# Kernel optimization log

Measured on AMD Instinct MI355X. Metric: run time of the kernel, lower is better.

## Reference

```python
import jax, jax.numpy as jnp
import numpy as np

N_NODES = 100000
N_EDGES = 1000000
D_FEAT = 128
N_ACTIONS = 64


def setup_inputs() -> dict:
    key = jax.random.key(0)
    ks = jax.random.split(key, 8)
    return {
        "x": jax.random.normal(ks[0], (N_NODES, D_FEAT), dtype=jnp.float32),
        "edge_index": jax.random.randint(ks[1], (2, N_EDGES), 0, N_NODES, dtype=jnp.int64),
        "W_gcn": jax.random.normal(ks[2], (D_FEAT, D_FEAT), dtype=jnp.float32) / np.sqrt(D_FEAT),
        "b_gcn": jax.random.normal(ks[3], (D_FEAT,), dtype=jnp.float32) * 0.02,
        "W_high": jax.random.normal(ks[4], (D_FEAT, N_ACTIONS), dtype=jnp.float32) / np.sqrt(D_FEAT),
        "b_high": jax.random.normal(ks[5], (N_ACTIONS,), dtype=jnp.float32) * 0.02,
        "W_low": jax.random.normal(ks[6], (D_FEAT, N_ACTIONS), dtype=jnp.float32) / np.sqrt(D_FEAT),
        "b_low": jax.random.normal(ks[7], (N_ACTIONS,), dtype=jnp.float32) * 0.02,
    }


def gcn_conv(x, edge_index, W, b):
    """PyG GCNConv: add self-loops, symmetric normalization, aggregate, linear."""
    n = x.shape[0]
    loops = jnp.arange(n, dtype=edge_index.dtype)
    src = jnp.concatenate([edge_index[0], loops])  # message sources
    dst = jnp.concatenate([edge_index[1], loops])  # message targets
    # degree of each target node (edge weight 1, incl. self-loop)
    deg = jax.ops.segment_sum(jnp.ones(src.shape[0], dtype=x.dtype), dst, num_segments=n)
    dinv = jax.lax.rsqrt(deg)  # deg >= 1 thanks to self-loops
    norm = dinv[src] * dinv[dst]  # [E+N]
    h = x @ W  # [N, D] dense transform first (cheaper than transforming messages)
    agg = jax.ops.segment_sum(h[src] * norm[:, None], dst, num_segments=n)
    return agg + b


def reference(x, edge_index, W_gcn, b_gcn, W_high, b_high, W_low, b_low):
    h = gcn_conv(x, edge_index, W_gcn, b_gcn)  # [N, D]
    high = h @ W_high + b_high  # [N, A]
    low = h @ W_low + b_low     # [N, A]
    return (high, low)
```

## Files before the change

### kernel.cpp

```cpp
#include <hip/hip_runtime.h>


#define BLOCK 256
#define SB 512
#define NB_MAX 784
#define SLOT 2048
#define CHUNK_MAX 2048

typedef _Float16 half8 __attribute__((ext_vector_type(8)));
typedef _Float16 half4 __attribute__((ext_vector_type(4)));
typedef float f32x4 __attribute__((ext_vector_type(4)));


__global__ __launch_bounds__(BLOCK) void k_prep(const float* __restrict__ Wg,
                                                const float* __restrict__ Wh,
                                                const float* __restrict__ Wl,
                                                const float* __restrict__ bg,
                                                const float* __restrict__ bh,
                                                const float* __restrict__ bl,
                                                _Float16* __restrict__ WfT,
                                                float* __restrict__ bf,
                                                int* __restrict__ cursor,
                                                int NB) {
    int b = blockIdx.x;
    if (b < 16) {
        int r = b * 8 + (threadIdx.x >> 5);
        int c0 = (threadIdx.x & 31) * 4;
        float a0 = 0.f, a1 = 0.f, a2 = 0.f, a3 = 0.f;
        for (int j = 0; j < 128; j++) {
            float wg = Wg[r * 128 + j];
            float4 wc;
            if (c0 < 64) wc = *(const float4*)(Wh + j * 64 + c0);
            else         wc = *(const float4*)(Wl + j * 64 + (c0 - 64));
            a0 += wg * wc.x; a1 += wg * wc.y; a2 += wg * wc.z; a3 += wg * wc.w;
        }
        WfT[(size_t)(c0 + 0) * 128 + r] = (_Float16)a0;
        WfT[(size_t)(c0 + 1) * 128 + r] = (_Float16)a1;
        WfT[(size_t)(c0 + 2) * 128 + r] = (_Float16)a2;
        WfT[(size_t)(c0 + 3) * 128 + r] = (_Float16)a3;
    } else {
        int c = threadIdx.x;
        if (c < 128) {
            float acc = (c < 64) ? bh[c] : bl[c - 64];
            for (int j = 0; j < 128; j++) {
                float wc = (c < 64) ? Wh[j * 64 + c] : Wl[j * 64 + (c - 64)];
                acc += bg[j] * wc;
            }
            bf[c] = acc;
        }
        for (int i = threadIdx.x; i < NB; i += BLOCK) cursor[i] = i * SLOT;
    }
}


__global__ __launch_bounds__(BLOCK) void k_scatter(const int* __restrict__ src,
                                                   const int* __restrict__ dst, int E,
                                                   int* __restrict__ cursor,
                                                   int2* __restrict__ ebuf, int NB) {
    __shared__ int2 stash[CHUNK_MAX];
    __shared__ int hist[NB_MAX];
    __shared__ int cur[NB_MAX];
    int blk = blockIdx.x;
    int chunk = (E + SB - 1) / SB;
    int e0 = blk * chunk, e1 = min(E, e0 + chunk);
    int m = e1 - e0;

    for (int i = threadIdx.x; i < NB; i += BLOCK) hist[i] = 0;
    __syncthreads();
    for (int i = threadIdx.x; i < m; i += BLOCK) {
        int d = dst[e0 + i], s = src[e0 + i];
        stash[i] = make_int2(d, s);
        atomicAdd(&hist[d >> 7], 1);
    }
    __syncthreads();
    for (int i = threadIdx.x; i < NB; i += BLOCK) {
        int h = hist[i];
        cur[i] = h ? atomicAdd(&cursor[i], h) : 0;
    }
    __syncthreads();
    for (int i = threadIdx.x; i < m; i += BLOCK) {
        int2 p = stash[i];
        int pos = atomicAdd(&cur[p.x >> 7], 1);
        ebuf[pos] = p;
    }
}


__global__ __launch_bounds__(BLOCK) void k_node(const int2* __restrict__ ebuf,
                                                const int* __restrict__ cursor,
                                                const float* __restrict__ x,
                                                int2* __restrict__ off2,
                                                float* __restrict__ dinv,
                                                int* __restrict__ csr,
                                                _Float16* __restrict__ xh,
                                                int n) {
    __shared__ int cnt[128];
    __shared__ int pre[128];
    __shared__ int cur[128];
    int bkt = blockIdx.x;
    int t = threadIdx.x;
    int node0 = bkt << 7;
    int nn = min(128, n - node0);
    int eb0 = bkt * SLOT;
    int eb1 = cursor[bkt];

    if (t < 128) cnt[t] = 0;
    __syncthreads();
    for (int e = eb0 + t; e < eb1; e += BLOCK)
        atomicAdd(&cnt[ebuf[e].x & 127], 1);
    __syncthreads();
    if (t < 128) pre[t] = cnt[t];
    __syncthreads();
    for (int ofs = 1; ofs < 128; ofs <<= 1) {
        int v = (t < 128 && t >= ofs) ? pre[t - ofs] : 0;
        __syncthreads();
        if (t < 128) pre[t] += v;
        __syncthreads();
    }
    if (t < 128) cur[t] = pre[t] - cnt[t];
    __syncthreads();
    if (t < nn) {
        off2[node0 + t] = make_int2(eb0 + cur[t], eb0 + pre[t]);
        dinv[node0 + t] = rsqrtf((float)(cnt[t] + 1));
    }
    for (int e = eb0 + t; e < eb1; e += BLOCK) {
        int2 p = ebuf[e];
        int pos = atomicAdd(&cur[p.x & 127], 1);
        csr[eb0 + pos] = p.y;
    }
    const float4* xr = (const float4*)(x + (size_t)node0 * 128);
    half4* xw = (half4*)(xh + (size_t)node0 * 128);
    for (int idx = t; idx < nn * 32; idx += BLOCK) {
        int row = idx >> 5;
        float dvL = rsqrtf((float)(cnt[row] + 1));
        float4 v = xr[idx];
        half4 o;
        o.x = (_Float16)(dvL * v.x); o.y = (_Float16)(dvL * v.y);
        o.z = (_Float16)(dvL * v.z); o.w = (_Float16)(dvL * v.w);
        xw[idx] = o;
    }
}


__global__ __launch_bounds__(BLOCK) void k_gf(const int2* __restrict__ off2,
                                              const int* __restrict__ csr,
                                              const float* __restrict__ dinv,
                                              const _Float16* __restrict__ xh,
                                              const _Float16* __restrict__ WfT,
                                              const float* __restrict__ bf,
                                              float* __restrict__ out, int n) {
    __shared__ _Float16 lds[64 * 128];
    int wave = threadIdx.x >> 6;
    int lane = threadIdx.x & 63;
    int g = lane >> 4;
    int sl = lane & 15;
    int T0 = blockIdx.x * 64;
    int wrow0 = wave * 16;
    int lbase = g << 4;

    for (int p = 0; p < 4; p++) {
        int r = wrow0 + p * 4 + g;
        int d = T0 + r;
        int dc = min(d, n - 1);
        int2 oe = off2[dc];
        float dv = dinv[dc];
        int beg = oe.x;
        int end = (d < n) ? oe.y : oe.x;
        half8 sv = *(const half8*)(xh + (size_t)dc * 128 + sl * 8);
        float acc[8];
#pragma unroll
        for (int k = 0; k < 8; k++) acc[k] = (float)sv[k];

        for (int b0 = beg; b0 < end; b0 += 16) {
            int take = min(16, end - b0);
            int s = 0;
            if (sl < take) s = csr[b0 + sl];
            for (int j = 0; j < take; j += 4) {
                int se0 = __shfl(s, lbase + j);
                int se1 = __shfl(s, lbase + ((j + 1) & 15));
                int se2 = __shfl(s, lbase + ((j + 2) & 15));
                int se3 = __shfl(s, lbase + ((j + 3) & 15));
                float m1 = (j + 1 < take) ? 1.f : 0.f;
                float m2 = (j + 2 < take) ? 1.f : 0.f;
                float m3 = (j + 3 < take) ? 1.f : 0.f;
                half8 v0 = *(const half8*)(xh + (size_t)se0 * 128 + sl * 8);
                half8 v1 = *(const half8*)(xh + (size_t)se1 * 128 + sl * 8);
                half8 v2 = *(const half8*)(xh + (size_t)se2 * 128 + sl * 8);
                half8 v3 = *(const half8*)(xh + (size_t)se3 * 128 + sl * 8);
#pragma unroll
                for (int k = 0; k < 8; k++)
                    acc[k] += (float)v0[k] + m1 * (float)v1[k]
                            + m2 * (float)v2[k] + m3 * (float)v3[k];
            }
        }
        half8 o;
#pragma unroll
        for (int k = 0; k < 8; k++) o[k] = (_Float16)(dv * acc[k]);
        *(half8*)(lds + (size_t)r * 128 + ((sl ^ (r & 7)) * 8)) = o;
    }

    int l15 = sl, lk = g;
    half8 a[4];
    {
        int r = wrow0 + l15;
#pragma unroll
        for (int kk = 0; kk < 4; kk++) {
            int ch = (kk * 4 + lk) ^ (l15 & 7);
            a[kk] = *(const half8*)(lds + (size_t)r * 128 + ch * 8);
        }
    }
    f32x4 acc[8];
#pragma unroll
    for (int cf = 0; cf < 8; cf++) acc[cf] = (f32x4){0.f, 0.f, 0.f, 0.f};
#pragma unroll
    for (int kk = 0; kk < 4; kk++) {
#pragma unroll
        for (int cf = 0; cf < 8; cf++) {
            half8 bfr = *(const half8*)(WfT + (size_t)(cf * 16 + l15) * 128 + kk * 32 + lk * 8);
            acc[cf] = __builtin_amdgcn_mfma_f32_16x16x32_f16(a[kk], bfr, acc[cf], 0, 0, 0);
        }
    }
#pragma unroll
    for (int cf = 0; cf < 8; cf++) {
        int c = cf * 16 + l15;
        float bv = bf[c];
        size_t cbase = (c < 64) ? (size_t)c : (size_t)n * 64 + (size_t)(c - 64);
        int r0 = T0 + wrow0 + lk * 4;
#pragma unroll
        for (int j = 0; j < 4; j++) {
            int rr = r0 + j;
            if (rr < n) out[cbase + (size_t)rr * 64] = acc[cf][j] + bv;
        }
    }
}

extern "C" void kernel_launch(void* const* d_in, const int* in_sizes, int n_in,
                              void* d_out, int out_size, void* d_ws, size_t ws_size,
                              hipStream_t stream) {
    const float* x  = (const float*)d_in[0];
    const int*   ei = (const int*)d_in[1];
    const float* Wg = (const float*)d_in[2];
    const float* bg = (const float*)d_in[3];
    const float* Wh = (const float*)d_in[4];
    const float* bh = (const float*)d_in[5];
    const float* Wl = (const float*)d_in[6];
    const float* bl = (const float*)d_in[7];
    float* out = (float*)d_out;

    int n = in_sizes[0] / 128;
    int E = in_sizes[1] / 2;
    const int* src = ei;
    const int* dst = ei + E;
    int NB = (n + 127) >> 7;

#define WS_TAKE(ptr, type, count)                                        \
    ptr = (type*)wsp;                                                    \
    wsp = (char*)(((size_t)(wsp + (size_t)(count) * sizeof(type)) + 255) \
                  & ~(size_t)255)

    char* wsp = (char*)d_ws;
    int*      cursor; WS_TAKE(cursor, int,      NB_MAX);
    int2*     ebuf;   WS_TAKE(ebuf,   int2,     (size_t)NB_MAX * SLOT);
    int2*     off2;   WS_TAKE(off2,   int2,     n);
    float*    dinv;   WS_TAKE(dinv,   float,    n);
    int*      csr;    WS_TAKE(csr,    int,      (size_t)NB_MAX * SLOT);
    _Float16* WfT;    WS_TAKE(WfT,    _Float16, 128 * 128);
    float*    bf;     WS_TAKE(bf,     float,    128);
    _Float16* xh;     WS_TAKE(xh,     _Float16, (size_t)n * 128);

    k_prep<<<17, BLOCK, 0, stream>>>(Wg, Wh, Wl, bg, bh, bl, WfT, bf, cursor, NB);
    k_scatter<<<SB, BLOCK, 0, stream>>>(src, dst, E, cursor, ebuf, NB);
    k_node<<<NB, BLOCK, 0, stream>>>(ebuf, cursor, x, off2, dinv, csr, xh, n);
    k_gf<<<(n + 63) / 64, BLOCK, 0, stream>>>(off2, csr, dinv, xh, WfT, bf, out, n);
}
```

Measured before the change: 245.3 us.

## Fuse prep into scatter, pack edges, restructure gather to wave-per-node

Merges the weight-prep kernel into the scatter kernel and initializes cursors with a memset. Edge records are packed into one int (src plus local dst in the high bits), which halves the bucket buffer traffic, and the dinv array is dropped in favour of recomputing rsqrt from the degree. The aggregation now gives each node a whole 64-lane wave that reads 2 halves per lane, uses readlane to broadcast neighbor indices, and prefetches the next node's CSR chunk. The packing assumes node ids fit in 20 bits, and the wider per-node gather may waste lanes on low-degree nodes.

```diff
diff --git a/kernel.cpp b/kernel.cpp
--- a/kernel.cpp
+++ b/kernel.cpp
@@ -5,23 +5,20 @@
 #define SB 512
 #define NB_MAX 784
 #define SLOT 2048
-#define CHUNK_MAX 2048
 
 typedef _Float16 half8 __attribute__((ext_vector_type(8)));
 typedef _Float16 half4 __attribute__((ext_vector_type(4)));
+typedef _Float16 half2v __attribute__((ext_vector_type(2)));
 typedef float f32x4 __attribute__((ext_vector_type(4)));
 
 
-__global__ __launch_bounds__(BLOCK) void k_prep(const float* __restrict__ Wg,
-                                                const float* __restrict__ Wh,
-                                                const float* __restrict__ Wl,
-                                                const float* __restrict__ bg,
-                                                const float* __restrict__ bh,
-                                                const float* __restrict__ bl,
-                                                _Float16* __restrict__ WfT,
-                                                float* __restrict__ bf,
-                                                int* __restrict__ cursor,
-                                                int NB) {
+__global__ __launch_bounds__(BLOCK) void k_scatter(
+    const int* __restrict__ src, const int* __restrict__ dst, int E,
+    const float* __restrict__ Wg, const float* __restrict__ Wh,
+    const float* __restrict__ Wl, const float* __restrict__ bg,
+    const float* __restrict__ bh, const float* __restrict__ bl,
+    _Float16* __restrict__ WfT, float* __restrict__ bf,
+    int* __restrict__ cursor, int* __restrict__ ebuf, int NB) {
     int b = blockIdx.x;
     if (b < 16) {
         int r = b * 8 + (threadIdx.x >> 5);
@@ -38,7 +35,7 @@
         WfT[(size_t)(c0 + 1) * 128 + r] = (_Float16)a1;
         WfT[(size_t)(c0 + 2) * 128 + r] = (_Float16)a2;
         WfT[(size_t)(c0 + 3) * 128 + r] = (_Float16)a3;
-    } else {
+    } else if (b == 16) {
         int c = threadIdx.x;
         if (c < 128) {
             float acc = (c < 64) ? bh[c] : bl[c - 64];
@@ -48,49 +45,35 @@
             }
             bf[c] = acc;
         }
-        for (int i = threadIdx.x; i < NB; i += BLOCK) cursor[i] = i * SLOT;
-    }
-}
-
-
-__global__ __launch_bounds__(BLOCK) void k_scatter(const int* __restrict__ src,
-                                                   const int* __restrict__ dst, int E,
-                                                   int* __restrict__ cursor,
-                                                   int2* __restrict__ ebuf, int NB) {
-    __shared__ int2 stash[CHUNK_MAX];
-    __shared__ int hist[NB_MAX];
-    __shared__ int cur[NB_MAX];
-    int blk = blockIdx.x;
-    int chunk = (E + SB - 1) / SB;
-    int e0 = blk * chunk, e1 = min(E, e0 + chunk);
-    int m = e1 - e0;
-
-    for (int i = threadIdx.x; i < NB; i += BLOCK) hist[i] = 0;
-    __syncthreads();
-    for (int i = threadIdx.x; i < m; i += BLOCK) {
-        int d = dst[e0 + i], s = src[e0 + i];
-        stash[i] = make_int2(d, s);
-        atomicAdd(&hist[d >> 7], 1);
-    }
-    __syncthreads();
-    for (int i = threadIdx.x; i < NB; i += BLOCK) {
-        int h = hist[i];
-        cur[i] = h ? atomicAdd(&cursor[i], h) : 0;
-    }
-    __syncthreads();
-    for (int i = threadIdx.x; i < m; i += BLOCK) {
-        int2 p = stash[i];
-        int pos = atomicAdd(&cur[p.x >> 7], 1);
-        ebuf[pos] = p;
-    }
-}
-
-
-__global__ __launch_bounds__(BLOCK) void k_node(const int2* __restrict__ ebuf,
+    } else {
+        __shared__ int hist[NB_MAX];
+        __shared__ int cur[NB_MAX];
+        int blk = b - 17;
+        int chunk = (E + SB - 1) / SB;
+        int e0 = blk * chunk, e1 = min(E, e0 + chunk);
+        for (int i = threadIdx.x; i < NB; i += BLOCK) hist[i] = 0;
+        __syncthreads();
+        for (int e = e0 + threadIdx.x; e < e1; e += BLOCK)
+            atomicAdd(&hist[dst[e] >> 7], 1);
+        __syncthreads();
+        for (int i = threadIdx.x; i < NB; i += BLOCK) {
+            int h = hist[i];
+            cur[i] = i * SLOT + (h ? atomicAdd(&cursor[i], h) : 0);
+        }
+        __syncthreads();
+        for (int e = e0 + threadIdx.x; e < e1; e += BLOCK) {
+            int d = dst[e], s = src[e];
+            int pos = atomicAdd(&cur[d >> 7], 1);
+            ebuf[pos] = s | ((d & 127) << 20);
+        }
+    }
+}
+
+
+__global__ __launch_bounds__(BLOCK) void k_node(const int* __restrict__ ebuf,
                                                 const int* __restrict__ cursor,
                                                 const float* __restrict__ x,
                                                 int2* __restrict__ off2,
-                                                float* __restrict__ dinv,
                                                 int* __restrict__ csr,
                                                 _Float16* __restrict__ xh,
                                                 int n) {
@@ -102,12 +85,12 @@
     int node0 = bkt << 7;
     int nn = min(128, n - node0);
     int eb0 = bkt * SLOT;
-    int eb1 = cursor[bkt];
+    int eb1 = eb0 + cursor[bkt];
 
     if (t < 128) cnt[t] = 0;
     __syncthreads();
     for (int e = eb0 + t; e < eb1; e += BLOCK)
-        atomicAdd(&cnt[ebuf[e].x & 127], 1);
+        atomicAdd(&cnt[(ebuf[e] >> 20) & 127], 1);
     __syncthreads();
     if (t < 128) pre[t] = cnt[t];
     __syncthreads();
@@ -119,14 +102,12 @@
     }
     if (t < 128) cur[t] = pre[t] - cnt[t];
     __syncthreads();
-    if (t < nn) {
+    if (t < nn)
         off2[node0 + t] = make_int2(eb0 + cur[t], eb0 + pre[t]);
-        dinv[node0 + t] = rsqrtf((float)(cnt[t] + 1));
-    }
     for (int e = eb0 + t; e < eb1; e += BLOCK) {
-        int2 p = ebuf[e];
-        int pos = atomicAdd(&cur[p.x & 127], 1);
-        csr[eb0 + pos] = p.y;
+        int p = ebuf[e];
+        int pos = atomicAdd(&cur[(p >> 20) & 127], 1);
+        csr[eb0 + pos] = p & 0xFFFFF;
     }
     const float4* xr = (const float4*)(x + (size_t)node0 * 128);
     half4* xw = (half4*)(xh + (size_t)node0 * 128);
@@ -144,7 +125,6 @@
 
 __global__ __launch_bounds__(BLOCK) void k_gf(const int2* __restrict__ off2,
                                               const int* __restrict__ csr,
-                                              const float* __restrict__ dinv,
                                               const _Float16* __restrict__ xh,
                                               const _Float16* __restrict__ WfT,
                                               const float* __restrict__ bf,
@@ -152,54 +132,67 @@
     __shared__ _Float16 lds[64 * 128];
     int wave = threadIdx.x >> 6;
     int lane = threadIdx.x & 63;
-    int g = lane >> 4;
-    int sl = lane & 15;
     int T0 = blockIdx.x * 64;
     int wrow0 = wave * 16;
-    int lbase = g << 4;
-
-    for (int p = 0; p < 4; p++) {
-        int r = wrow0 + p * 4 + g;
-        int d = T0 + r;
-        int dc = min(d, n - 1);
-        int2 oe = off2[dc];
-        float dv = dinv[dc];
-        int beg = oe.x;
-        int end = (d < n) ? oe.y : oe.x;
-        half8 sv = *(const half8*)(xh + (size_t)dc * 128 + sl * 8);
-        float acc[8];
-#pragma unroll
-        for (int k = 0; k < 8; k++) acc[k] = (float)sv[k];
-
-        for (int b0 = beg; b0 < end; b0 += 16) {
-            int take = min(16, end - b0);
-            int s = 0;
-            if (sl < take) s = csr[b0 + sl];
-            for (int j = 0; j < take; j += 4) {
-                int se0 = __shfl(s, lbase + j);
-                int se1 = __shfl(s, lbase + ((j + 1) & 15));
-                int se2 = __shfl(s, lbase + ((j + 2) & 15));
-                int se3 = __shfl(s, lbase + ((j + 3) & 15));
-                float m1 = (j + 1 < take) ? 1.f : 0.f;
-                float m2 = (j + 2 < take) ? 1.f : 0.f;
-                float m3 = (j + 3 < take) ? 1.f : 0.f;
-                half8 v0 = *(const half8*)(xh + (size_t)se0 * 128 + sl * 8);
-                half8 v1 = *(const half8*)(xh + (size_t)se1 * 128 + sl * 8);
-                half8 v2 = *(const half8*)(xh + (size_t)se2 * 128 + sl * 8);
-                half8 v3 = *(const half8*)(xh + (size_t)se3 * 128 + sl * 8);
-#pragma unroll
-                for (int k = 0; k < 8; k++)
-                    acc[k] += (float)v0[k] + m1 * (float)v1[k]
-                            + m2 * (float)v2[k] + m3 * (float)v3[k];
+    int nbase = T0 + wrow0;
+
+    int pidx = min(nbase + (lane & 15), n - 1);
+    int2 oe = off2[pidx];
+
+    int sb_cur;
+    {
+        int beg0 = __builtin_amdgcn_readlane(oe.x, 0);
+        sb_cur = csr[beg0 + lane];
+    }
+
+    for (int i = 0; i < 16; i++) {
+        int inext = (i + 1) & 15;
+        int begn = __builtin_amdgcn_readlane(oe.x, inext);
+        int sb_next = csr[begn + lane];
+
+        int beg = __builtin_amdgcn_readlane(oe.x, i);
+        int end = __builtin_amdgcn_readlane(oe.y, i);
+        int deg = end - beg;
+        float dv = rsqrtf((float)(deg + 1));
+
+        int r = wrow0 + i;
+        int d = min(T0 + r, n - 1);
+        half2v sv = ((const half2v*)(xh + (size_t)d * 128))[lane];
+        float ax = (float)sv.x, ay = (float)sv.y;
+
+        int b0 = 0;
+        do {
+            int sb = (b0 == 0) ? sb_cur : csr[beg + b0 + lane];
+            int nb = min(64, deg - b0);
+            for (int rb = 0; rb < nb; rb += 8) {
+                half2v v[8];
+                float m[8];
+#pragma unroll
+                for (int j = 0; j < 8; j++) {
+                    int se = __builtin_amdgcn_readlane(sb, rb + j);
+                    se = min(max(se, 0), n - 1);
+                    v[j] = ((const half2v*)(xh + (size_t)se * 128))[lane];
+                    m[j] = (rb + j < nb) ? 1.f : 0.f;
+                }
+#pragma unroll
+                for (int j = 0; j < 8; j++) {
+                    ax += m[j] * (float)v[j].x;
+                    ay += m[j] * (float)v[j].y;
+                }
             }
-        }
-        half8 o;
-#pragma unroll
-        for (int k = 0; k < 8; k++) o[k] = (_Float16)(dv * acc[k]);
-        *(half8*)(lds + (size_t)r * 128 + ((sl ^ (r & 7)) * 8)) = o;
-    }
-
-    int l15 = sl, lk = g;
+            b0 += 64;
+        } while (b0 < deg);
+        sb_cur = sb_next;
+
+        half2v o;
+        o.x = (_Float16)(dv * ax);
+        o.y = (_Float16)(dv * ay);
+        int c = lane >> 2;
+        int off_h = (((c ^ (r & 7)) << 3) + ((lane & 3) << 1));
+        *(half2v*)(lds + r * 128 + off_h) = o;
+    }
+
+    int l15 = lane & 15, lk = lane >> 4;
     half8 a[4];
     {
         int r = wrow0 + l15;
@@ -260,16 +253,16 @@
 
     char* wsp = (char*)d_ws;
     int*      cursor; WS_TAKE(cursor, int,      NB_MAX);
-    int2*     ebuf;   WS_TAKE(ebuf,   int2,     (size_t)NB_MAX * SLOT);
+    int*      ebuf;   WS_TAKE(ebuf,   int,      (size_t)NB_MAX * SLOT);
     int2*     off2;   WS_TAKE(off2,   int2,     n);
-    float*    dinv;   WS_TAKE(dinv,   float,    n);
     int*      csr;    WS_TAKE(csr,    int,      (size_t)NB_MAX * SLOT);
     _Float16* WfT;    WS_TAKE(WfT,    _Float16, 128 * 128);
     float*    bf;     WS_TAKE(bf,     float,    128);
     _Float16* xh;     WS_TAKE(xh,     _Float16, (size_t)n * 128);
 
-    k_prep<<<17, BLOCK, 0, stream>>>(Wg, Wh, Wl, bg, bh, bl, WfT, bf, cursor, NB);
-    k_scatter<<<SB, BLOCK, 0, stream>>>(src, dst, E, cursor, ebuf, NB);
-    k_node<<<NB, BLOCK, 0, stream>>>(ebuf, cursor, x, off2, dinv, csr, xh, n);
-    k_gf<<<(n + 63) / 64, BLOCK, 0, stream>>>(off2, csr, dinv, xh, WfT, bf, out, n);
-}
+    hipMemsetAsync(cursor, 0, (size_t)NB * 4, stream);
+    k_scatter<<<17 + SB, BLOCK, 0, stream>>>(
+        src, dst, E, Wg, Wh, Wl, bg, bh, bl, WfT, bf, cursor, ebuf, NB);
+    k_node<<<NB, BLOCK, 0, stream>>>(ebuf, cursor, x, off2, csr, xh, n);
+    k_gf<<<(n + 63) / 64, BLOCK, 0, stream>>>(off2, csr, xh, WfT, bf, out, n);
+}
```

Measured after the change: 248.4 us. No clear change (+1.3%).
